# Kernel tuning notes

Measured on AMD Instinct MI355X. Metric: run time of the kernel, lower is better.

## Reference

```python
import jax, jax.numpy as jnp
import numpy as np

V, E, H, T = 30000, 512, 512, 32
B, L = 64, 512


def setup_inputs() -> dict:
    key = jax.random.key(0)
    ks = jax.random.split(key, 14)
    n = lambda k, shape: (jax.random.normal(k, shape, jnp.float32) * 0.05)
    return {
        "x": jax.random.randint(ks[0], (B, L), 0, V),
        "embedding": n(ks[1], (V, E)),
        # PyTorch LSTM params, gate order (i, f, g, o); biases b_ih+b_hh fused
        "w_ih_f": n(ks[2], (4 * H, E)),
        "w_hh_f": n(ks[3], (4 * H, H)),
        "b_f": n(ks[4], (4 * H,)),
        "w_ih_b": n(ks[5], (4 * H, E)),
        "w_hh_b": n(ks[6], (4 * H, H)),
        "b_b": n(ks[7], (4 * H,)),
        "W": n(ks[8], (T, 2 * H)),
        "b": n(ks[9], (T,)),
        # CRF params (torchcrf)
        "start": n(ks[10], (T,)),
        "end": n(ks[11], (T,)),
        "trans": n(ks[12], (T, T)),
    }


def _lstm(x, w_ih, w_hh, bias):
    # x: [L, B, E] -> hidden states [L, B, H]; PyTorch gate equations
    h_dim = w_hh.shape[1]
    xp = jnp.einsum('lbe,ge->lbg', x, w_ih) + bias  # precompute input proj [L,B,4H]

    def step(carry, xt):
        h, c = carry
        g = xt + h @ w_hh.T
        i, f, gg, o = jnp.split(g, 4, axis=-1)
        c = jax.nn.sigmoid(f) * c + jax.nn.sigmoid(i) * jnp.tanh(gg)
        h = jax.nn.sigmoid(o) * jnp.tanh(c)
        return (h, c), h

    bsz = x.shape[1]
    init = (jnp.zeros((bsz, h_dim), x.dtype), jnp.zeros((bsz, h_dim), x.dtype))
    _, hs = jax.lax.scan(step, init, xp)
    return hs


def _emissions(x, embedding, w_ih_f, w_hh_f, b_f, w_ih_b, w_hh_b, b_b, W, b):
    emb = embedding[x]                      # [B, L, E]
    xt = jnp.transpose(emb, (1, 0, 2))      # [L, B, E]
    hf = _lstm(xt, w_ih_f, w_hh_f, b_f)     # [L, B, H]
    hb = _lstm(xt[::-1], w_ih_b, w_hh_b, b_b)[::-1]
    h = jnp.concatenate([hf, hb], axis=-1)  # [L, B, 2H]
    return h @ W.T + b                      # [L, B, T]


def _viterbi(em, start, end, trans):
    # em: [L, B, T]; torchcrf CRF.decode with no mask (all timesteps valid)
    score = start + em[0]                   # [B, T]

    def step(score, em_t):
        nxt = score[:, :, None] + trans[None] + em_t[:, None, :]  # [B, T_prev, T_cur]
        return jnp.max(nxt, axis=1), jnp.argmax(nxt, axis=1)

    score, hist = jax.lax.scan(step, score, em[1:])  # hist: [L-1, B, T]
    score = score + end
    last = jnp.argmax(score, axis=-1)       # [B]

    def back(tag, idx_t):
        prev = jnp.take_along_axis(idx_t, tag[:, None], axis=1)[:, 0]
        return prev, prev

    _, prevs = jax.lax.scan(back, last, hist, reverse=True)  # [L-1, B]
    tags = jnp.concatenate([prevs, last[None]], axis=0)      # [L, B]
    return tags.T.astype(jnp.int32)                          # [B, L]


def reference(x, embedding, w_ih_f, w_hh_f, b_f, w_ih_b, w_hh_b, b_b, W, b, start, end, trans):
    em = _emissions(x, embedding, w_ih_f, w_hh_f, b_f, w_ih_b, w_hh_b, b_b, W, b)
    return _viterbi(em, start, end, trans)
```

## Files before the change

kernel.cpp:

```cpp
#include <hip/hip_runtime.h>
#include <cstdio>
#include <cstdint>


typedef float f32x4 __attribute__((ext_vector_type(4)));
typedef float f32x2 __attribute__((ext_vector_type(2)));

#define PKFMA(ACC, W2, H2) \
    asm("v_pk_fma_f32 %0, %1, %2, %0" : "+v"(ACC) : "v"(W2), "v"(H2))

__global__ __launch_bounds__(512) void k_gather(
    const int* __restrict__ x, const float* __restrict__ emb,
    float4* __restrict__ eg4)
{
    const int t   = blockIdx.x;
    const int tid = threadIdx.x;
    __shared__ int xv[64];
    if (tid < 64) xv[tid] = x[tid * 512 + t];
    __syncthreads();
    #pragma unroll
    for (int i = 0; i < 16; ++i) {
        const int flat = i * 512 + tid;
        const int b  = flat & 63;
        const int e4 = flat >> 6;
        const float4 v = *reinterpret_cast<const float4*>(
            emb + (size_t)xv[b] * 512 + e4 * 4);
        eg4[((size_t)t * 128 + e4) * 64 + b] = v;
    }
}

__global__ __launch_bounds__(256) void k_pack(
    const float* __restrict__ wih_f, const float* __restrict__ whh_f,
    const float* __restrict__ wih_b, const float* __restrict__ whh_b,
    float* __restrict__ wpack)
{
    const int i = blockIdx.x * 256 + threadIdx.x;
    const int j   = i & 3;
    const int r   = (i >> 2) & 7;
    const int kc  = (i >> 5) & 15;
    const int sec = (i >> 9) & 1;
    const int ks  = (i >> 10) & 7;
    const int wg  = (i >> 13) & 255;
    const int dir = (i >> 21) & 1;
    const int k   = ks * 64 + kc * 4 + j;
    const int g   = r >> 1, colL = r & 1;
    const int rg  = g * 512 + wg * 2 + colL;
    const float* wih = dir ? wih_b : wih_f;
    const float* whh = dir ? whh_b : whh_f;
    const float v = sec ? whh[(size_t)rg * 512 + k] : wih[(size_t)rg * 512 + k];
    wpack[i] = v;
}

__global__ __launch_bounds__(512, 2) void k_lstm(
    const float4* __restrict__ eg4, const float* __restrict__ wpack,
    const float* __restrict__ b_f, const float* __restrict__ b_b,
    float* __restrict__ h_f, float* __restrict__ h_b,
    int* __restrict__ bar)
{
    const int bid = blockIdx.x;
    const int dir = bid >> 8;
    const int wg  = bid & 255;
    float* HH       = dir ? h_b : h_f;
    const float* BS = dir ? b_b : b_f;
    int* flg = bar + (size_t)dir * 131072;

    const int tid = threadIdx.x;
    const int b   = tid & 63;
    const int ks  = __builtin_amdgcn_readfirstlane(tid >> 6);

    __shared__ float wlds[8][1024];
    __shared__ float partb[8 * 8 * 64];
    __shared__ float hlds[64][2];

    {
        const float4* src = reinterpret_cast<const float4*>(
            wpack + (size_t)((dir * 256 + wg) * 8 + ks) * 1024);
        float4* dst = reinterpret_cast<float4*>(&wlds[ks][0]);
        #pragma unroll
        for (int i = 0; i < 4; ++i)
            dst[i * 64 + b] = src[i * 64 + b];
    }

    const int colL = (tid >> 6) & 1;
    float bias4[4] = {0.f, 0.f, 0.f, 0.f};
    if (tid < 128) {
        #pragma unroll
        for (int g = 0; g < 4; ++g) bias4[g] = BS[g * 512 + wg * 2 + colL];
    }
    float cst = 0.f;
    __syncthreads();

    const float* wl = &wlds[ks][0];

    f32x2 eacc2[8];
    #pragma unroll
    for (int r = 0; r < 8; ++r) eacc2[r] = (f32x2){0.f, 0.f};

    {
        const int t0 = dir ? 511 : 0;
        const float4* ep = eg4 + ((size_t)t0 * 128 + ks * 16) * 64 + b;
        #pragma unroll
        for (int half = 0; half < 2; ++half) {
            f32x4 v[8];
            #pragma unroll
            for (int kc = 0; kc < 8; ++kc)
                v[kc] = *reinterpret_cast<const f32x4*>(ep + (size_t)(half * 8 + kc) * 64);
            #pragma unroll
            for (int kc = 0; kc < 8; ++kc) {
                const float* wp = wl + (half * 8 + kc) * 32;
                const f32x2 elo = __builtin_shufflevector(v[kc], v[kc], 0, 1);
                const f32x2 ehi = __builtin_shufflevector(v[kc], v[kc], 2, 3);
                #pragma unroll
                for (int r = 0; r < 8; ++r) {
                    const f32x4 w4 = *reinterpret_cast<const f32x4*>(wp + r * 4);
                    const f32x2 wlo = __builtin_shufflevector(w4, w4, 0, 1);
                    const f32x2 whi = __builtin_shufflevector(w4, w4, 2, 3);
                    PKFMA(eacc2[r], wlo, elo);
                    PKFMA(eacc2[r], whi, ehi);
                }
            }
        }
    }

    for (int s = 0; s < 512; ++s) {
        const int t = dir ? (511 - s) : s;
        f32x2 acc2[8];
        #pragma unroll
        for (int r = 0; r < 8; ++r) acc2[r] = eacc2[r];

        if (s > 0) {
            const int* fp = flg + (size_t)(s - 1) * 256 + ks * 32 + (b & 31);
            while (__hip_atomic_load(fp, __ATOMIC_RELAXED,
                                     __HIP_MEMORY_SCOPE_AGENT) == 0)
                __builtin_amdgcn_s_sleep(1);

            const int tp = dir ? (t + 1) : (t - 1);
            const f32x2* hq = reinterpret_cast<const f32x2*>(HH)
                              + ((size_t)tp * 256 + ks * 32) * 64 + b;
            #pragma unroll
            for (int half = 0; half < 2; ++half) {
                f32x2 hv[16];
                #pragma unroll
                for (int kq = 0; kq < 16; ++kq)
                    hv[kq] = hq[(size_t)(half * 16 + kq) * 64];
                #pragma unroll
                for (int kc = 0; kc < 8; ++kc) {
                    const float* wp = wl + 512 + (half * 8 + kc) * 32;
                    #pragma unroll
                    for (int r = 0; r < 8; ++r) {
                        const f32x4 w4 = *reinterpret_cast<const f32x4*>(wp + r * 4);
                        const f32x2 wlo = __builtin_shufflevector(w4, w4, 0, 1);
                        const f32x2 whi = __builtin_shufflevector(w4, w4, 2, 3);
                        PKFMA(acc2[r], wlo, hv[kc * 2]);
                        PKFMA(acc2[r], whi, hv[kc * 2 + 1]);
                    }
                }
            }
        }

        #pragma unroll
        for (int r = 0; r < 8; ++r)
            partb[(ks * 8 + r) * 64 + b] = acc2[r][0] + acc2[r][1];
        __syncthreads();

        if (tid < 128) {
            float g4[4];
            #pragma unroll
            for (int g = 0; g < 4; ++g) {
                const int r = g * 2 + colL;
                float v = bias4[g];
                #pragma unroll
                for (int w = 0; w < 8; ++w) v += partb[(w * 8 + r) * 64 + b];
                g4[g] = v;
            }
            const float si = 1.f / (1.f + expf(-g4[0]));
            const float sf = 1.f / (1.f + expf(-g4[1]));
            const float tg = tanhf(g4[2]);
            const float so = 1.f / (1.f + expf(-g4[3]));
            cst = sf * cst + si * tg;
            hlds[b][colL] = so * tanhf(cst);
        }
        __syncthreads();

        if (tid < 64) {
            f32x2 o;
            o[0] = hlds[tid][0]; o[1] = hlds[tid][1];
            float* dst = HH + (((size_t)t * 256 + wg) * 64 + tid) * 2;
            asm volatile("global_store_dwordx2 %0, %1, off sc1"
                         :: "v"(dst), "v"(o) : "memory");
            asm volatile("s_waitcnt vmcnt(0)" ::: "memory");
            if (tid == 0 && s < 511)
                __hip_atomic_store(flg + (size_t)s * 256 + wg, 1,
                                   __ATOMIC_RELAXED, __HIP_MEMORY_SCOPE_AGENT);
        }

        if (s < 511) {
            const int tn = dir ? (t - 1) : (t + 1);
            const float4* ep = eg4 + ((size_t)tn * 128 + ks * 16) * 64 + b;
            #pragma unroll
            for (int r = 0; r < 8; ++r) eacc2[r] = (f32x2){0.f, 0.f};
            #pragma unroll
            for (int half = 0; half < 2; ++half) {
                f32x4 v[8];
                #pragma unroll
                for (int kc = 0; kc < 8; ++kc)
                    v[kc] = *reinterpret_cast<const f32x4*>(ep + (size_t)(half * 8 + kc) * 64);
                #pragma unroll
                for (int kc = 0; kc < 8; ++kc) {
                    const float* wp = wl + (half * 8 + kc) * 32;
                    const f32x2 elo = __builtin_shufflevector(v[kc], v[kc], 0, 1);
                    const f32x2 ehi = __builtin_shufflevector(v[kc], v[kc], 2, 3);
                    #pragma unroll
                    for (int r = 0; r < 8; ++r) {
                        const f32x4 w4 = *reinterpret_cast<const f32x4*>(wp + r * 4);
                        const f32x2 wlo = __builtin_shufflevector(w4, w4, 0, 1);
                        const f32x2 whi = __builtin_shufflevector(w4, w4, 2, 3);
                        PKFMA(eacc2[r], wlo, elo);
                        PKFMA(eacc2[r], whi, ehi);
                    }
                }
            }
        }
    }
}

__global__ __launch_bounds__(256) void k_em(
    const float* __restrict__ hf, const float* __restrict__ hb,
    const float* __restrict__ Wm, const float* __restrict__ bias,
    float* __restrict__ em)
{
    const int t   = blockIdx.x;
    const int tid = threadIdx.x;
    const int b   = tid & 63;
    const int tg  = tid >> 6;
    __shared__ float Wl[128][33];
    float acc[8] = {};

    for (int ch = 0; ch < 8; ++ch) {
        {
            const int tag = tid >> 3;
            const int kq  = tid & 7;
            const float* src = Wm + (size_t)tag * 1024 + ch * 128 + kq * 16;
            #pragma unroll
            for (int ii = 0; ii < 4; ++ii) {
                const float4 v = *reinterpret_cast<const float4*>(src + ii * 4);
                const int k0 = kq * 16 + ii * 4;
                Wl[k0 + 0][tag] = v.x; Wl[k0 + 1][tag] = v.y;
                Wl[k0 + 2][tag] = v.z; Wl[k0 + 3][tag] = v.w;
            }
        }
        __syncthreads();
        const f32x2* hsrc2 = (ch < 4)
            ? (reinterpret_cast<const f32x2*>(hf) + ((size_t)t * 256 + ch * 64) * 64 + b)
            : (reinterpret_cast<const f32x2*>(hb) + ((size_t)t * 256 + (ch - 4) * 64) * 64 + b);
        #pragma unroll 4
        for (int c2l = 0; c2l < 64; ++c2l) {
            const f32x2 h2 = hsrc2[(size_t)c2l * 64];
            #pragma unroll
            for (int j = 0; j < 2; ++j)
                #pragma unroll
                for (int jt = 0; jt < 8; ++jt)
                    acc[jt] = fmaf(h2[j], Wl[c2l * 2 + j][tg * 8 + jt], acc[jt]);
        }
        __syncthreads();
    }

    #pragma unroll
    for (int jt = 0; jt < 8; ++jt) {
        const int tag = tg * 8 + jt;
        em[((size_t)t * 64 + b) * 32 + tag] = acc[jt] + bias[tag];
    }
}

__global__ __launch_bounds__(64) void k_vit(
    const float* __restrict__ em, const float* __restrict__ startv,
    const float* __restrict__ endv, const float* __restrict__ trans,
    int* __restrict__ out)
{
    const int b    = blockIdx.x;
    const int lane = threadIdx.x;
    const int c    = lane & 31;
    const bool act = lane < 32;
    __shared__ unsigned char hist[511][32];
    __shared__ int outb[512];

    float tr[32];
    #pragma unroll 8
    for (int p = 0; p < 32; ++p) tr[p] = trans[p * 32 + c];

    float s = act ? (startv[c] + em[(size_t)b * 32 + c]) : -1e30f;

    for (int t = 1; t < 512; ++t) {
        const float emc = act ? em[((size_t)t * 64 + b) * 32 + c] : 0.f;
        float m = -1e30f; int arg = 0;
        #pragma unroll 8
        for (int p = 0; p < 32; ++p) {
            const float v = __shfl(s, p) + tr[p] + emc;
            if (v > m) { m = v; arg = p; }
        }
        if (act) { s = m; hist[t - 1][c] = (unsigned char)arg; }
    }

    s = act ? (s + endv[c]) : -1e30f;
    int idx = act ? c : 63;
    #pragma unroll
    for (int off = 32; off >= 1; off >>= 1) {
        const float om = __shfl_down(s, off);
        const int   oi = __shfl_down(idx, off);
        if (om > s || (om == s && oi < idx)) { s = om; idx = oi; }
    }
    idx = __shfl(idx, 0);

    if (lane == 0) {
        int tag = idx;
        outb[511] = tag;
        for (int t = 510; t >= 0; --t) { tag = hist[t][tag]; outb[t] = tag; }
    }
    __syncthreads();
    for (int i = lane; i < 512; i += 64) out[(size_t)b * 512 + i] = outb[i];
}

extern "C" void kernel_launch(void* const* d_in, const int* in_sizes, int n_in,
                              void* d_out, int out_size, void* d_ws, size_t ws_size,
                              hipStream_t stream)
{
    const int*   x      = (const int*)d_in[0];
    const float* emb    = (const float*)d_in[1];
    const float* w_ih_f = (const float*)d_in[2];
    const float* w_hh_f = (const float*)d_in[3];
    const float* b_f    = (const float*)d_in[4];
    const float* w_ih_b = (const float*)d_in[5];
    const float* w_hh_b = (const float*)d_in[6];
    const float* b_b    = (const float*)d_in[7];
    const float* Wm     = (const float*)d_in[8];
    const float* bvec   = (const float*)d_in[9];
    const float* startv = (const float*)d_in[10];
    const float* endv   = (const float*)d_in[11];
    const float* trans  = (const float*)d_in[12];
    int* out = (int*)d_out;

    float* ws    = (float*)d_ws;
    float* eg    = ws;
    float* h_f   = ws + 16777216;
    float* h_b   = ws + 33554432;
    float* em    = ws + 50331648;
    float* wpack = ws + 51380224;
    int*   bar   = (int*)(ws + 55574528);

    const size_t need = (size_t)(55574528 + 262144) * 4;
    if (ws_size < need) {
        fprintf(stderr, "kernel_launch: ws too small: %zu < %zu\n", ws_size, need);
        return;
    }

    (void)hipMemsetAsync(bar, 0, 1048576, stream);
    k_gather<<<dim3(512),   512, 0, stream>>>(x, emb, (float4*)eg);
    k_pack  <<<dim3(16384), 256, 0, stream>>>(w_ih_f, w_hh_f, w_ih_b, w_hh_b, wpack);
    k_lstm  <<<dim3(512),   512, 0, stream>>>((const float4*)eg, wpack, b_f, b_b,
                                              h_f, h_b, bar);
    k_em    <<<dim3(512),   256, 0, stream>>>(h_f, h_b, Wm, bvec, em);
    k_vit   <<<dim3(64),     64, 0, stream>>>(em, startv, endv, trans, out);
}
```

Baseline: 6.391 ms.

## Specialize LSTM waves: recurrent matvec vs input projection running concurrently

Splits the 8 waves of each LSTM block into two roles. Four waves do only the recurrent h@W_hh product, with W_hh in LDS. The other four compute the next step's input projection from global memory and also do the gate nonlinearities and the h store. The goal is to take the input-projection work and the extra barrier off the serial critical path, using double-buffered partial sums. It also moves to per-column-pair flags polled with a 64-bit load, and drops the second LDS hop for the h store. The cost is that input-projection weights are now read from global memory every step.

```diff
diff --git a/kernel.cpp b/kernel.cpp
--- a/kernel.cpp
+++ b/kernel.cpp
@@ -51,6 +51,38 @@
     wpack[i] = v;
 }
 
+__device__ __forceinline__ void edot128(
+    const float4* __restrict__ eg4, const float* __restrict__ wpackbase,
+    const int t, const int sl, const int b, f32x2 eacc2[8])
+{
+    #pragma unroll
+    for (int r = 0; r < 8; ++r) eacc2[r] = (f32x2){0.f, 0.f};
+    #pragma unroll
+    for (int c = 0; c < 4; ++c) {
+        f32x4 v[8];
+        #pragma unroll
+        for (int kc = 0; kc < 8; ++kc)
+            v[kc] = *reinterpret_cast<const f32x4*>(
+                eg4 + ((size_t)t * 128 + sl * 32 + c * 8 + kc) * 64 + b);
+        const float* wp0 = wpackbase + (size_t)(2 * sl + (c >> 1)) * 1024
+                           + (c & 1) * 256;
+        #pragma unroll
+        for (int kc = 0; kc < 8; ++kc) {
+            const float* wp = wp0 + kc * 32;
+            const f32x2 elo = __builtin_shufflevector(v[kc], v[kc], 0, 1);
+            const f32x2 ehi = __builtin_shufflevector(v[kc], v[kc], 2, 3);
+            #pragma unroll
+            for (int r = 0; r < 8; ++r) {
+                const f32x4 w4 = *reinterpret_cast<const f32x4*>(wp + r * 4);
+                const f32x2 wlo = __builtin_shufflevector(w4, w4, 0, 1);
+                const f32x2 whi = __builtin_shufflevector(w4, w4, 2, 3);
+                PKFMA(eacc2[r], wlo, elo);
+                PKFMA(eacc2[r], whi, ehi);
+            }
+        }
+    }
+}
+
 __global__ __launch_bounds__(512, 2) void k_lstm(
     const float4* __restrict__ eg4, const float* __restrict__ wpack,
     const float* __restrict__ b_f, const float* __restrict__ b_b,
@@ -62,115 +94,106 @@
     const int wg  = bid & 255;
     float* HH       = dir ? h_b : h_f;
     const float* BS = dir ? b_b : b_f;
-    int* flg = bar + (size_t)dir * 131072;
+    int* flg = bar + (size_t)dir * 262144;
 
     const int tid = threadIdx.x;
     const int b   = tid & 63;
-    const int ks  = __builtin_amdgcn_readfirstlane(tid >> 6);
-
-    __shared__ float wlds[8][1024];
-    __shared__ float partb[8 * 8 * 64];
-    __shared__ float hlds[64][2];
-
-    {
-        const float4* src = reinterpret_cast<const float4*>(
-            wpack + (size_t)((dir * 256 + wg) * 8 + ks) * 1024);
-        float4* dst = reinterpret_cast<float4*>(&wlds[ks][0]);
+    const int wid = __builtin_amdgcn_readfirstlane(tid >> 6);
+    const int sl  = wid & 3;
+
+    __shared__ float wlds[4][1024];
+    __shared__ float partb[2][8][8][64];
+
+    const float* wpbase = wpack + (size_t)(dir * 256 + wg) * 8192;
+
+    if (wid < 4) {
         #pragma unroll
-        for (int i = 0; i < 4; ++i)
-            dst[i * 64 + b] = src[i * 64 + b];
-    }
-
-    const int colL = (tid >> 6) & 1;
+        for (int q = 0; q < 2; ++q) {
+            const float4* src = reinterpret_cast<const float4*>(
+                wpbase + (size_t)(2 * sl + q) * 1024 + 512);
+            float4* dst = reinterpret_cast<float4*>(&wlds[sl][q * 512]);
+            #pragma unroll
+            for (int i = 0; i < 2; ++i)
+                dst[i * 64 + b] = src[i * 64 + b];
+        }
+    }
+
+    const int l    = tid - 256;
+    const int colL = l & 1;
+    const int gb   = l >> 1;
     float bias4[4] = {0.f, 0.f, 0.f, 0.f};
-    if (tid < 128) {
+    float cst = 0.f;
+    if (wid == 4 || wid == 5) {
         #pragma unroll
         for (int g = 0; g < 4; ++g) bias4[g] = BS[g * 512 + wg * 2 + colL];
     }
-    float cst = 0.f;
+
+    f32x2 eacc2[8];
+    #pragma unroll
+    for (int r = 0; r < 8; ++r) eacc2[r] = (f32x2){0.f, 0.f};
+    if (wid >= 4) {
+        const int t0 = dir ? 511 : 0;
+        edot128(eg4, wpbase, t0, sl, b, eacc2);
+    }
     __syncthreads();
-
-    const float* wl = &wlds[ks][0];
-
-    f32x2 eacc2[8];
-    #pragma unroll
-    for (int r = 0; r < 8; ++r) eacc2[r] = (f32x2){0.f, 0.f};
-
-    {
-        const int t0 = dir ? 511 : 0;
-        const float4* ep = eg4 + ((size_t)t0 * 128 + ks * 16) * 64 + b;
-        #pragma unroll
-        for (int half = 0; half < 2; ++half) {
-            f32x4 v[8];
-            #pragma unroll
-            for (int kc = 0; kc < 8; ++kc)
-                v[kc] = *reinterpret_cast<const f32x4*>(ep + (size_t)(half * 8 + kc) * 64);
-            #pragma unroll
-            for (int kc = 0; kc < 8; ++kc) {
-                const float* wp = wl + (half * 8 + kc) * 32;
-                const f32x2 elo = __builtin_shufflevector(v[kc], v[kc], 0, 1);
-                const f32x2 ehi = __builtin_shufflevector(v[kc], v[kc], 2, 3);
-                #pragma unroll
-                for (int r = 0; r < 8; ++r) {
-                    const f32x4 w4 = *reinterpret_cast<const f32x4*>(wp + r * 4);
-                    const f32x2 wlo = __builtin_shufflevector(w4, w4, 0, 1);
-                    const f32x2 whi = __builtin_shufflevector(w4, w4, 2, 3);
-                    PKFMA(eacc2[r], wlo, elo);
-                    PKFMA(eacc2[r], whi, ehi);
-                }
-            }
-        }
-    }
 
     for (int s = 0; s < 512; ++s) {
         const int t = dir ? (511 - s) : s;
-        f32x2 acc2[8];
-        #pragma unroll
-        for (int r = 0; r < 8; ++r) acc2[r] = eacc2[r];
-
-        if (s > 0) {
-            const int* fp = flg + (size_t)(s - 1) * 256 + ks * 32 + (b & 31);
-            while (__hip_atomic_load(fp, __ATOMIC_RELAXED,
-                                     __HIP_MEMORY_SCOPE_AGENT) == 0)
-                __builtin_amdgcn_s_sleep(1);
-
-            const int tp = dir ? (t + 1) : (t - 1);
-            const f32x2* hq = reinterpret_cast<const f32x2*>(HH)
-                              + ((size_t)tp * 256 + ks * 32) * 64 + b;
-            #pragma unroll
-            for (int half = 0; half < 2; ++half) {
-                f32x2 hv[16];
+
+        if (wid < 4) {
+            f32x2 acc2[8];
+            #pragma unroll
+            for (int r = 0; r < 8; ++r) acc2[r] = (f32x2){0.f, 0.f};
+            if (s > 0) {
+                const long long* fp = reinterpret_cast<const long long*>(
+                    flg + (size_t)(s - 1) * 512 + sl * 128) + b;
+                while (__hip_atomic_load(fp, __ATOMIC_RELAXED,
+                                         __HIP_MEMORY_SCOPE_AGENT)
+                       != 0x0000000100000001LL)
+                    __builtin_amdgcn_s_sleep(1);
+
+                const int tp = dir ? (t + 1) : (t - 1);
+                const f32x2* hq = reinterpret_cast<const f32x2*>(HH)
+                                  + ((size_t)tp * 256 + sl * 64) * 64 + b;
                 #pragma unroll
-                for (int kq = 0; kq < 16; ++kq)
-                    hv[kq] = hq[(size_t)(half * 16 + kq) * 64];
-                #pragma unroll
-                for (int kc = 0; kc < 8; ++kc) {
-                    const float* wp = wl + 512 + (half * 8 + kc) * 32;
+                for (int c = 0; c < 4; ++c) {
+                    f32x2 hv[16];
                     #pragma unroll
-                    for (int r = 0; r < 8; ++r) {
-                        const f32x4 w4 = *reinterpret_cast<const f32x4*>(wp + r * 4);
-                        const f32x2 wlo = __builtin_shufflevector(w4, w4, 0, 1);
-                        const f32x2 whi = __builtin_shufflevector(w4, w4, 2, 3);
-                        PKFMA(acc2[r], wlo, hv[kc * 2]);
-                        PKFMA(acc2[r], whi, hv[kc * 2 + 1]);
+                    for (int kq = 0; kq < 16; ++kq)
+                        hv[kq] = hq[(size_t)(c * 16 + kq) * 64];
+                    #pragma unroll
+                    for (int kc = 0; kc < 8; ++kc) {
+                        const float* wp = &wlds[sl][c * 256 + kc * 32];
+                        #pragma unroll
+                        for (int r = 0; r < 8; ++r) {
+                            const f32x4 w4 = *reinterpret_cast<const f32x4*>(wp + r * 4);
+                            const f32x2 wlo = __builtin_shufflevector(w4, w4, 0, 1);
+                            const f32x2 whi = __builtin_shufflevector(w4, w4, 2, 3);
+                            PKFMA(acc2[r], wlo, hv[kc * 2]);
+                            PKFMA(acc2[r], whi, hv[kc * 2 + 1]);
+                        }
                     }
                 }
             }
-        }
-
-        #pragma unroll
-        for (int r = 0; r < 8; ++r)
-            partb[(ks * 8 + r) * 64 + b] = acc2[r][0] + acc2[r][1];
+            #pragma unroll
+            for (int r = 0; r < 8; ++r)
+                partb[s & 1][sl][r][b] = acc2[r][0] + acc2[r][1];
+        } else {
+            #pragma unroll
+            for (int r = 0; r < 8; ++r)
+                partb[s & 1][4 + sl][r][b] = eacc2[r][0] + eacc2[r][1];
+        }
+
         __syncthreads();
 
-        if (tid < 128) {
+        if (wid == 4 || wid == 5) {
             float g4[4];
             #pragma unroll
             for (int g = 0; g < 4; ++g) {
                 const int r = g * 2 + colL;
                 float v = bias4[g];
                 #pragma unroll
-                for (int w = 0; w < 8; ++w) v += partb[(w * 8 + r) * 64 + b];
+                for (int w = 0; w < 8; ++w) v += partb[s & 1][w][r][gb];
                 g4[g] = v;
             }
             const float si = 1.f / (1.f + expf(-g4[0]));
@@ -178,48 +201,19 @@
             const float tg = tanhf(g4[2]);
             const float so = 1.f / (1.f + expf(-g4[3]));
             cst = sf * cst + si * tg;
-            hlds[b][colL] = so * tanhf(cst);
-        }
-        __syncthreads();
-
-        if (tid < 64) {
-            f32x2 o;
-            o[0] = hlds[tid][0]; o[1] = hlds[tid][1];
-            float* dst = HH + (((size_t)t * 256 + wg) * 64 + tid) * 2;
-            asm volatile("global_store_dwordx2 %0, %1, off sc1"
-                         :: "v"(dst), "v"(o) : "memory");
+            const float hval = so * tanhf(cst);
+            float* dst = HH + ((size_t)t * 256 + wg) * 128 + l;
+            asm volatile("global_store_dword %0, %1, off sc1"
+                         :: "v"(dst), "v"(hval) : "memory");
             asm volatile("s_waitcnt vmcnt(0)" ::: "memory");
-            if (tid == 0 && s < 511)
-                __hip_atomic_store(flg + (size_t)s * 256 + wg, 1,
+            if ((l == 0 || l == 64) && s < 511)
+                __hip_atomic_store(flg + (size_t)s * 512 + wg * 2 + (l >> 6), 1,
                                    __ATOMIC_RELAXED, __HIP_MEMORY_SCOPE_AGENT);
         }
 
-        if (s < 511) {
-            const int tn = dir ? (t - 1) : (t + 1);
-            const float4* ep = eg4 + ((size_t)tn * 128 + ks * 16) * 64 + b;
-            #pragma unroll
-            for (int r = 0; r < 8; ++r) eacc2[r] = (f32x2){0.f, 0.f};
-            #pragma unroll
-            for (int half = 0; half < 2; ++half) {
-                f32x4 v[8];
-                #pragma unroll
-                for (int kc = 0; kc < 8; ++kc)
-                    v[kc] = *reinterpret_cast<const f32x4*>(ep + (size_t)(half * 8 + kc) * 64);
-                #pragma unroll
-                for (int kc = 0; kc < 8; ++kc) {
-                    const float* wp = wl + (half * 8 + kc) * 32;
-                    const f32x2 elo = __builtin_shufflevector(v[kc], v[kc], 0, 1);
-                    const f32x2 ehi = __builtin_shufflevector(v[kc], v[kc], 2, 3);
-                    #pragma unroll
-                    for (int r = 0; r < 8; ++r) {
-                        const f32x4 w4 = *reinterpret_cast<const f32x4*>(wp + r * 4);
-                        const f32x2 wlo = __builtin_shufflevector(w4, w4, 0, 1);
-                        const f32x2 whi = __builtin_shufflevector(w4, w4, 2, 3);
-                        PKFMA(eacc2[r], wlo, elo);
-                        PKFMA(eacc2[r], whi, ehi);
-                    }
-                }
-            }
+        if (wid >= 4 && s < 511) {
+            const int tn = dir ? (510 - s) : (s + 1);
+            edot128(eg4, wpbase, tn, sl, b, eacc2);
         }
     }
 }
@@ -347,13 +341,13 @@
     float* wpack = ws + 51380224;
     int*   bar   = (int*)(ws + 55574528);
 
-    const size_t need = (size_t)(55574528 + 262144) * 4;
+    const size_t need = (size_t)(55574528 + 524288) * 4;
     if (ws_size < need) {
         fprintf(stderr, "kernel_launch: ws too small: %zu < %zu\n", ws_size, need);
         return;
     }
 
-    (void)hipMemsetAsync(bar, 0, 1048576, stream);
+    (void)hipMemsetAsync(bar, 0, 2097152, stream);
     k_gather<<<dim3(512),   512, 0, stream>>>(x, emb, (float4*)eg);
     k_pack  <<<dim3(16384), 256, 0, stream>>>(w_ih_f, w_hh_f, w_ih_b, w_hh_b, wpack);
     k_lstm  <<<dim3(512),   512, 0, stream>>>((const float4*)eg, wpack, b_f, b_b,
```

Result: slower. 10.75 ms (+68.1%).
